# Optimization experiments

Hardware: AMD Instinct MI355X
Metric: run time of the kernel (lower is better)

Reference implementation:

```python
import jax, jax.numpy as jnp
import numpy as np

D_REDUCE = 32
# combination indices (i<j), lexicographic, matching torch.combinations
_IDX_I, _IDX_J = np.triu_indices(D_REDUCE, k=1)


def setup_inputs() -> dict:
    key = jax.random.key(0)
    ks = jax.random.split(key, 5)
    B, L, d_model, d_red = 8, 4096, 1024, D_REDUCE
    plucker_dim = d_red * (d_red - 1) // 2  # 496
    return {
        "h": jax.random.normal(ks[0], (B, L, d_model), dtype=jnp.float32),
        "window_offset": 1,
        "W_red_w": jax.random.normal(ks[1], (d_model, d_red), dtype=jnp.float32) * (1.0 / np.sqrt(d_model)),
        "W_red_b": jax.random.normal(ks[2], (d_red,), dtype=jnp.float32) * 0.01,
        "W_plu_w": jax.random.normal(ks[3], (plucker_dim, d_model), dtype=jnp.float32) * (1.0 / np.sqrt(plucker_dim)),
        "W_plu_b": jax.random.normal(ks[4], (d_model,), dtype=jnp.float32) * 0.01,
    }


def reference(h, window_offset, W_red_w, W_red_b, W_plu_w, W_plu_b):
    B, L, d_model = h.shape
    delta = int(window_offset)
    if delta >= L:
        return jnp.zeros_like(h)
    idx_i = jnp.asarray(_IDX_I)
    idx_j = jnp.asarray(_IDX_J)
    # reduce: (B, L, d_red)
    z = jnp.einsum("bld,dr->blr", h, W_red_w) + W_red_b
    z_t = z[:, delta:, :]        # (B, L-delta, d_red)
    z_td = z[:, : L - delta, :]  # (B, L-delta, d_red)
    # Plucker coordinates: p_ij = z_t[i]*z_td[j] - z_t[j]*z_td[i]  -> (B, L-delta, 496)
    p = z_t[..., idx_i] * z_td[..., idx_j] - z_t[..., idx_j] * z_td[..., idx_i]
    norm = jnp.sqrt(jnp.sum(p * p, axis=-1, keepdims=True))
    p_hat = p / jnp.maximum(norm, 1e-8)
    g_valid = jnp.einsum("blp,pd->bld", p_hat, W_plu_w) + W_plu_b
    g = jnp.zeros((B, L, d_model), dtype=h.dtype)
    g = g.at[:, delta:, :].set(g_valid)
    return g
```

## Files before the change

kernel.cpp:

```cpp
#include <hip/hip_runtime.h>
#include <hip/hip_bf16.h>

#define L_SEQ  4096
#define NBATCH 8
#define DMODEL 1024
#define DRED   32
#define NPAIR  496
#define PK     512
#define MROWS  (NBATCH * L_SEQ)

typedef __bf16 bf16x8 __attribute__((ext_vector_type(8)));
typedef float  f32x4  __attribute__((ext_vector_type(4)));
typedef unsigned short u16x8 __attribute__((ext_vector_type(8)));

typedef const __attribute__((address_space(1))) void g_void;
typedef __attribute__((address_space(3))) void lds_void;

struct PairTab { unsigned short v[512]; };
static constexpr PairTab make_tab() {
  PairTab t{};
  int p = 0;
  for (int i = 0; i < DRED; ++i)
    for (int j = i + 1; j < DRED; ++j) { t.v[p] = (unsigned short)(i | (j << 8)); ++p; }
  for (; p < 512; ++p) t.v[p] = 0;
  return t;
}
__constant__ PairTab PTAB = make_tab();

__global__ __launch_bounds__(256) void ktransW(const float* __restrict__ Wplu,
                                               __bf16* __restrict__ Wt) {
  __shared__ float tile[64][65];
  const int k0 = (blockIdx.x & 7) << 6;
  const int n0 = (blockIdx.x >> 3) << 6;
  const int tid = threadIdx.x;
#pragma unroll
  for (int it = 0; it < 16; ++it) {
    int e = it * 256 + tid;
    int i = e >> 6, j = e & 63;
    float v = 0.f;
    if (k0 + i < NPAIR) v = Wplu[(size_t)(k0 + i) * DMODEL + n0 + j];
    tile[i][j] = v;
  }
  __syncthreads();
#pragma unroll
  for (int it = 0; it < 16; ++it) {
    int e = it * 256 + tid;
    int rn = e >> 6, ck = e & 63;
    Wt[(size_t)(n0 + rn) * PK + k0 + ck] = (__bf16)tile[ck][rn];
  }
}

__global__ __launch_bounds__(256) void kprepWz(const float* __restrict__ Wred,
                                               __bf16* __restrict__ Bh,
                                               __bf16* __restrict__ Bl) {
  int idx = blockIdx.x * 256 + threadIdx.x;
  int n = idx >> 10, k = idx & 1023;
  float v = Wred[k * DRED + n];
  __bf16 hh = (__bf16)v;
  Bh[idx] = hh;
  Bl[idx] = (__bf16)(v - (float)hh);
}

__global__ __launch_bounds__(256) void kz(const float* __restrict__ h,
                                          const __bf16* __restrict__ Bh,
                                          const __bf16* __restrict__ Bl,
                                          const float* __restrict__ Wrb,
                                          float* __restrict__ z) {
  const int w = threadIdx.x >> 6;
  const int lane = threadIdx.x & 63;
  const int l15 = lane & 15, hi = lane >> 4;
  const int m0 = blockIdx.x * 64 + w * 16;
  f32x4 acc[2] = {};
  const float* hp = h + (size_t)(m0 + l15) * DMODEL + hi * 8;
  const __bf16* bh0 = Bh + (size_t)l15 * DMODEL + hi * 8;
  const __bf16* bh1 = bh0 + 16 * DMODEL;
  const __bf16* bl0 = Bl + (size_t)l15 * DMODEL + hi * 8;
  const __bf16* bl1 = bl0 + 16 * DMODEL;
#pragma unroll 8
  for (int kt = 0; kt < 32; ++kt) {
    const int ko = kt * 32;
    f32x4 v0 = *(const f32x4*)(hp + ko);
    f32x4 v1 = *(const f32x4*)(hp + ko + 4);
    bf16x8 ah, al;
#pragma unroll
    for (int q = 0; q < 4; ++q) {
      float f0 = v0[q], f1 = v1[q];
      __bf16 h0 = (__bf16)f0, h1 = (__bf16)f1;
      ah[q] = h0;     ah[q + 4] = h1;
      al[q] = (__bf16)(f0 - (float)h0);
      al[q + 4] = (__bf16)(f1 - (float)h1);
    }
    bf16x8 b0h = *(const bf16x8*)(bh0 + ko);
    bf16x8 b1h = *(const bf16x8*)(bh1 + ko);
    bf16x8 b0l = *(const bf16x8*)(bl0 + ko);
    bf16x8 b1l = *(const bf16x8*)(bl1 + ko);
    acc[0] = __builtin_amdgcn_mfma_f32_16x16x32_bf16(ah, b0h, acc[0], 0, 0, 0);
    acc[1] = __builtin_amdgcn_mfma_f32_16x16x32_bf16(ah, b1h, acc[1], 0, 0, 0);
    acc[0] = __builtin_amdgcn_mfma_f32_16x16x32_bf16(al, b0h, acc[0], 0, 0, 0);
    acc[1] = __builtin_amdgcn_mfma_f32_16x16x32_bf16(al, b1h, acc[1], 0, 0, 0);
    acc[0] = __builtin_amdgcn_mfma_f32_16x16x32_bf16(ah, b0l, acc[0], 0, 0, 0);
    acc[1] = __builtin_amdgcn_mfma_f32_16x16x32_bf16(ah, b1l, acc[1], 0, 0, 0);
  }
#pragma unroll
  for (int nt = 0; nt < 2; ++nt) {
    const float bias = Wrb[nt * 16 + l15];
#pragma unroll
    for (int q = 0; q < 4; ++q) {
      z[(size_t)(m0 + hi * 4 + q) * DRED + nt * 16 + l15] = acc[nt][q] + bias;
    }
  }
}

__global__ __launch_bounds__(256) void kpairs(const float* __restrict__ z,
                                              const int* __restrict__ dOff,
                                              __bf16* __restrict__ A) {
  const int delta = *dOff;
  const int lane = threadIdx.x & 63;
  const int m = blockIdx.x * 4 + (threadIdx.x >> 6);
  const int t = m & (L_SEQ - 1);
  __bf16* arow = A + (size_t)m * PK;
  if (t < delta) {
    u16x8 zz = {0, 0, 0, 0, 0, 0, 0, 0};
    *(u16x8*)(arow + lane * 8) = zz;
    return;
  }
  const float zt  = z[(size_t)m * DRED + (lane & 31)];
  const float ztd = z[(size_t)(m - delta) * DRED + (lane & 31)];
  const u16x8 tab = *(const u16x8*)(PTAB.v + lane * 8);
  float p[8];
  float s = 0.f;
#pragma unroll
  for (int q = 0; q < 8; ++q) {
    const int i = tab[q] & 255;
    const int j = tab[q] >> 8;
    float zti  = __shfl(zt,  i, 64);
    float ztdj = __shfl(ztd, j, 64);
    float ztj  = __shfl(zt,  j, 64);
    float ztdi = __shfl(ztd, i, 64);
    p[q] = fmaf(zti, ztdj, -(ztj * ztdi));
    s = fmaf(p[q], p[q], s);
  }
#pragma unroll
  for (int off = 1; off < 64; off <<= 1) s += __shfl_xor(s, off, 64);
  const float rcp = 1.f / fmaxf(sqrtf(s), 1e-8f);
  bf16x8 o;
#pragma unroll
  for (int q = 0; q < 8; ++q) o[q] = (__bf16)(p[q] * rcp);
  *(bf16x8*)(arow + lane * 8) = o;
}

__global__ __launch_bounds__(256) void kgemm(const __bf16* __restrict__ A,
                                             const __bf16* __restrict__ Bt,
                                             const float* __restrict__ bias,
                                             const int* __restrict__ dOff,
                                             float* __restrict__ out) {
  __shared__ __bf16 Asm[128 * 64];
  __shared__ __bf16 Bsm[128 * 64];
  const int delta = *dOff;
  const int d = blockIdx.x;
  const int lb = ((d & 7) << 8) + (d >> 3);
  const int bm = lb >> 3, bn = lb & 7;
  const int m0 = bm << 7, n0 = bn << 7;
  const int t = threadIdx.x;
  const int wv = t >> 6, lane = t & 63;
  const int l15 = lane & 15, hi = lane >> 4;
  const int wm = (wv >> 1) << 6, wn = (wv & 1) << 6;

  f32x4 acc[4][4] = {};

  for (int kt = 0; kt < 8; ++kt) {
    if (kt) __syncthreads();
    const int kbase = kt * 64;
#pragma unroll
    for (int it = 0; it < 4; ++it) {
      const int c = it * 256 + t;
      const int row = c >> 3, j = c & 7;
      const int jg = j ^ (row & 7);
      const __bf16* ga = A  + (size_t)(m0 + row) * PK + kbase + jg * 8;
      const __bf16* gb = Bt + (size_t)(n0 + row) * PK + kbase + jg * 8;
      char* la = (char*)Asm + (it * 256 + (wv << 6)) * 16;
      char* lbp = (char*)Bsm + (it * 256 + (wv << 6)) * 16;
      __builtin_amdgcn_global_load_lds((g_void*)ga, (lds_void*)la, 16, 0, 0);
      __builtin_amdgcn_global_load_lds((g_void*)gb, (lds_void*)lbp, 16, 0, 0);
    }
    __syncthreads();
#pragma unroll
    for (int kh = 0; kh < 2; ++kh) {
      bf16x8 afr[4], bfr[4];
#pragma unroll
      for (int mi = 0; mi < 4; ++mi) {
        const int row = wm + mi * 16 + l15;
        const int jj = (kh * 4 + hi) ^ (row & 7);
        afr[mi] = *(const bf16x8*)((const char*)Asm + row * 128 + jj * 16);
      }
#pragma unroll
      for (int ni = 0; ni < 4; ++ni) {
        const int row = wn + ni * 16 + l15;
        const int jj = (kh * 4 + hi) ^ (row & 7);
        bfr[ni] = *(const bf16x8*)((const char*)Bsm + row * 128 + jj * 16);
      }
#pragma unroll
      for (int mi = 0; mi < 4; ++mi)
#pragma unroll
        for (int ni = 0; ni < 4; ++ni)
          acc[mi][ni] = __builtin_amdgcn_mfma_f32_16x16x32_bf16(afr[mi], bfr[ni],
                                                                acc[mi][ni], 0, 0, 0);
    }
  }

  float bv[4];
#pragma unroll
  for (int ni = 0; ni < 4; ++ni) bv[ni] = bias[n0 + wn + ni * 16 + l15];
#pragma unroll
  for (int mi = 0; mi < 4; ++mi)
#pragma unroll
    for (int ni = 0; ni < 4; ++ni)
#pragma unroll
      for (int q = 0; q < 4; ++q) {
        const int row = m0 + wm + mi * 16 + hi * 4 + q;
        const int col = n0 + wn + ni * 16 + l15;
        float v = acc[mi][ni][q] + bv[ni];
        if ((row & (L_SEQ - 1)) < delta) v = 0.f;
        out[(size_t)row * DMODEL + col] = v;
      }
}

extern "C" void kernel_launch(void* const* d_in, const int* in_sizes, int n_in,
                              void* d_out, int out_size, void* d_ws, size_t ws_size,
                              hipStream_t stream) {
  const float* h    = (const float*)d_in[0];
  const int*   woff = (const int*)d_in[1];
  const float* Wred = (const float*)d_in[2];
  const float* Wrb  = (const float*)d_in[3];
  const float* Wplu = (const float*)d_in[4];
  const float* Wpb  = (const float*)d_in[5];
  float* out = (float*)d_out;

  char* ws = (char*)d_ws;
  float*  z   = (float*)ws;
  __bf16* Aph = (__bf16*)(ws + (4u << 20));
  __bf16* Wt  = (__bf16*)(ws + (36u << 20));
  __bf16* Bh  = (__bf16*)(ws + (37u << 20));
  __bf16* Bl  = (__bf16*)(ws + (37u << 20) + (64u << 10));

  hipLaunchKernelGGL(ktransW,  dim3(128),        dim3(256), 0, stream, Wplu, Wt);
  hipLaunchKernelGGL(kprepWz,  dim3(128),        dim3(256), 0, stream, Wred, Bh, Bl);
  hipLaunchKernelGGL(kz,       dim3(MROWS / 64), dim3(256), 0, stream, h, Bh, Bl, Wrb, z);
  hipLaunchKernelGGL(kpairs,   dim3(MROWS / 4),  dim3(256), 0, stream, z, woff, Aph);
  hipLaunchKernelGGL(kgemm,    dim3(2048),       dim3(256), 0, stream, Aph, Wt, Wpb, woff, out);
}
```

Measured before the change: 129.4 us.

## Double-buffer GEMM K-tiles in LDS to overlap global loads with MFMA

Splits the K loop of the Plucker GEMM into 32-wide tiles held in two LDS buffers. The next tile is prefetched with global_load_lds while MFMAs run on the current one, and the XOR swizzle is adjusted to the narrower row. This targets load latency that previously stalled each K step, at the cost of twice as many iterations and barriers. A risk is that __syncthreads may not wait on the async LDS loads.

```diff
diff --git a/kernel.cpp b/kernel.cpp
--- a/kernel.cpp
+++ b/kernel.cpp
@@ -154,8 +154,8 @@
                                              const float* __restrict__ bias,
                                              const int* __restrict__ dOff,
                                              float* __restrict__ out) {
-  __shared__ __bf16 Asm[128 * 64];
-  __shared__ __bf16 Bsm[128 * 64];
+  __shared__ __bf16 Asm[2][128 * 32];
+  __shared__ __bf16 Bsm[2][128 * 32];
   const int delta = *dOff;
   const int d = blockIdx.x;
   const int lb = ((d & 7) << 8) + (d >> 3);
@@ -168,45 +168,55 @@
 
   f32x4 acc[4][4] = {};
 
-  for (int kt = 0; kt < 8; ++kt) {
-    if (kt) __syncthreads();
-    const int kbase = kt * 64;
-#pragma unroll
-    for (int it = 0; it < 4; ++it) {
-      const int c = it * 256 + t;
-      const int row = c >> 3, j = c & 7;
-      const int jg = j ^ (row & 7);
-      const __bf16* ga = A  + (size_t)(m0 + row) * PK + kbase + jg * 8;
-      const __bf16* gb = Bt + (size_t)(n0 + row) * PK + kbase + jg * 8;
-      char* la = (char*)Asm + (it * 256 + (wv << 6)) * 16;
-      char* lbp = (char*)Bsm + (it * 256 + (wv << 6)) * 16;
-      __builtin_amdgcn_global_load_lds((g_void*)ga, (lds_void*)la, 16, 0, 0);
-      __builtin_amdgcn_global_load_lds((g_void*)gb, (lds_void*)lbp, 16, 0, 0);
-    }
+  const int r0 = t >> 2,         jsw0 = (t & 3) ^ (r0 & 3);
+  const int r1 = (t + 256) >> 2, jsw1 = (t & 3) ^ (r1 & 3);
+  const __bf16* gA0 = A  + (size_t)(m0 + r0) * PK + jsw0 * 8;
+  const __bf16* gA1 = A  + (size_t)(m0 + r1) * PK + jsw1 * 8;
+  const __bf16* gB0 = Bt + (size_t)(n0 + r0) * PK + jsw0 * 8;
+  const __bf16* gB1 = Bt + (size_t)(n0 + r1) * PK + jsw1 * 8;
+  const int cb0 = (wv << 6) * 16;
+  const int cb1 = (256 + (wv << 6)) * 16;
+
+#define STAGE(buf, kt) do {                                                          \
+    const int _ko = (kt) * 32;                                                       \
+    __builtin_amdgcn_global_load_lds((g_void*)(gA0 + _ko),                           \
+        (lds_void*)((char*)Asm[buf] + cb0), 16, 0, 0);                               \
+    __builtin_amdgcn_global_load_lds((g_void*)(gA1 + _ko),                           \
+        (lds_void*)((char*)Asm[buf] + cb1), 16, 0, 0);                               \
+    __builtin_amdgcn_global_load_lds((g_void*)(gB0 + _ko),                           \
+        (lds_void*)((char*)Bsm[buf] + cb0), 16, 0, 0);                               \
+    __builtin_amdgcn_global_load_lds((g_void*)(gB1 + _ko),                           \
+        (lds_void*)((char*)Bsm[buf] + cb1), 16, 0, 0);                               \
+  } while (0)
+
+  STAGE(0, 0);
+  __syncthreads();
+  int buf = 0;
+  for (int kt = 0; kt < 16; ++kt) {
+    if (kt < 15) STAGE(buf ^ 1, kt + 1);
+    bf16x8 afr[4], bfr[4];
+#pragma unroll
+    for (int mi = 0; mi < 4; ++mi) {
+      const int row = wm + mi * 16 + l15;
+      const int jj = hi ^ (row & 3);
+      afr[mi] = *(const bf16x8*)((const char*)Asm[buf] + row * 64 + jj * 16);
+    }
+#pragma unroll
+    for (int ni = 0; ni < 4; ++ni) {
+      const int row = wn + ni * 16 + l15;
+      const int jj = hi ^ (row & 3);
+      bfr[ni] = *(const bf16x8*)((const char*)Bsm[buf] + row * 64 + jj * 16);
+    }
+#pragma unroll
+    for (int mi = 0; mi < 4; ++mi)
+#pragma unroll
+      for (int ni = 0; ni < 4; ++ni)
+        acc[mi][ni] = __builtin_amdgcn_mfma_f32_16x16x32_bf16(afr[mi], bfr[ni],
+                                                              acc[mi][ni], 0, 0, 0);
     __syncthreads();
-#pragma unroll
-    for (int kh = 0; kh < 2; ++kh) {
-      bf16x8 afr[4], bfr[4];
-#pragma unroll
-      for (int mi = 0; mi < 4; ++mi) {
-        const int row = wm + mi * 16 + l15;
-        const int jj = (kh * 4 + hi) ^ (row & 7);
-        afr[mi] = *(const bf16x8*)((const char*)Asm + row * 128 + jj * 16);
-      }
-#pragma unroll
-      for (int ni = 0; ni < 4; ++ni) {
-        const int row = wn + ni * 16 + l15;
-        const int jj = (kh * 4 + hi) ^ (row & 7);
-        bfr[ni] = *(const bf16x8*)((const char*)Bsm + row * 128 + jj * 16);
-      }
-#pragma unroll
-      for (int mi = 0; mi < 4; ++mi)
-#pragma unroll
-        for (int ni = 0; ni < 4; ++ni)
-          acc[mi][ni] = __builtin_amdgcn_mfma_f32_16x16x32_bf16(afr[mi], bfr[ni],
-                                                                acc[mi][ni], 0, 0, 0);
-    }
-  }
+    buf ^= 1;
+  }
+#undef STAGE
 
   float bv[4];
 #pragma unroll
```

Result: slower. 132.9 us (+2.7%).

## Double-buffer LDS tiles in GEMM to overlap global loads with MFMA

Applied to the files above, without the earlier changes.

Splits the A/B shared-memory tiles into two buffers and prefetches the next K-tile with global_load_lds while MFMAs run on the current one. Uses explicit vmcnt waits and s_barrier in place of __syncthreads around each stage, and precomputes global pointers and LDS offsets outside the loop. This is meant to hide global-memory latency in the K loop, at the cost of doubling LDS use (64KB per block), which may reduce occupancy.

```diff
diff --git a/kernel.cpp b/kernel.cpp
--- a/kernel.cpp
+++ b/kernel.cpp
@@ -154,8 +154,8 @@
                                              const float* __restrict__ bias,
                                              const int* __restrict__ dOff,
                                              float* __restrict__ out) {
-  __shared__ __bf16 Asm[128 * 64];
-  __shared__ __bf16 Bsm[128 * 64];
+  __shared__ __bf16 Asm[2][128 * 64];
+  __shared__ __bf16 Bsm[2][128 * 64];
   const int delta = *dOff;
   const int d = blockIdx.x;
   const int lb = ((d & 7) << 8) + (d >> 3);
@@ -168,22 +168,39 @@
 
   f32x4 acc[4][4] = {};
 
+  const __bf16* gA[4];
+  const __bf16* gB[4];
+  int cb[4];
+#pragma unroll
+  for (int it = 0; it < 4; ++it) {
+    const int c = it * 256 + t;
+    const int row = c >> 3, j = t & 7;
+    const int jg = j ^ (row & 7);
+    gA[it] = A  + (size_t)(m0 + row) * PK + jg * 8;
+    gB[it] = Bt + (size_t)(n0 + row) * PK + jg * 8;
+    cb[it] = (it * 256 + (wv << 6)) * 16;
+  }
+
+#define STAGE(buf, kt) do {                                                      \
+    const int _ko = (kt) * 64;                                                   \
+    _Pragma("unroll")                                                            \
+    for (int _it = 0; _it < 4; ++_it) {                                          \
+      __builtin_amdgcn_global_load_lds((g_void*)(gA[_it] + _ko),                 \
+          (lds_void*)((char*)Asm[buf] + cb[_it]), 16, 0, 0);                     \
+      __builtin_amdgcn_global_load_lds((g_void*)(gB[_it] + _ko),                 \
+          (lds_void*)((char*)Bsm[buf] + cb[_it]), 16, 0, 0);                     \
+    }                                                                            \
+  } while (0)
+
+  STAGE(0, 0);
+#pragma unroll
   for (int kt = 0; kt < 8; ++kt) {
-    if (kt) __syncthreads();
-    const int kbase = kt * 64;
-#pragma unroll
-    for (int it = 0; it < 4; ++it) {
-      const int c = it * 256 + t;
-      const int row = c >> 3, j = c & 7;
-      const int jg = j ^ (row & 7);
-      const __bf16* ga = A  + (size_t)(m0 + row) * PK + kbase + jg * 8;
-      const __bf16* gb = Bt + (size_t)(n0 + row) * PK + kbase + jg * 8;
-      char* la = (char*)Asm + (it * 256 + (wv << 6)) * 16;
-      char* lbp = (char*)Bsm + (it * 256 + (wv << 6)) * 16;
-      __builtin_amdgcn_global_load_lds((g_void*)ga, (lds_void*)la, 16, 0, 0);
-      __builtin_amdgcn_global_load_lds((g_void*)gb, (lds_void*)lbp, 16, 0, 0);
-    }
-    __syncthreads();
+    const int buf = kt & 1;
+    if (kt < 7) STAGE(buf ^ 1, kt + 1);
+    if (kt < 7) asm volatile("s_waitcnt vmcnt(8)" ::: "memory");
+    else        asm volatile("s_waitcnt vmcnt(0)" ::: "memory");
+    __builtin_amdgcn_s_barrier();
+    __builtin_amdgcn_sched_barrier(0);
 #pragma unroll
     for (int kh = 0; kh < 2; ++kh) {
       bf16x8 afr[4], bfr[4];
@@ -191,13 +208,13 @@
       for (int mi = 0; mi < 4; ++mi) {
         const int row = wm + mi * 16 + l15;
         const int jj = (kh * 4 + hi) ^ (row & 7);
-        afr[mi] = *(const bf16x8*)((const char*)Asm + row * 128 + jj * 16);
+        afr[mi] = *(const bf16x8*)((const char*)Asm[buf] + row * 128 + jj * 16);
       }
 #pragma unroll
       for (int ni = 0; ni < 4; ++ni) {
         const int row = wn + ni * 16 + l15;
         const int jj = (kh * 4 + hi) ^ (row & 7);
-        bfr[ni] = *(const bf16x8*)((const char*)Bsm + row * 128 + jj * 16);
+        bfr[ni] = *(const bf16x8*)((const char*)Bsm[buf] + row * 128 + jj * 16);
       }
 #pragma unroll
       for (int mi = 0; mi < 4; ++mi)
@@ -206,7 +223,12 @@
           acc[mi][ni] = __builtin_amdgcn_mfma_f32_16x16x32_bf16(afr[mi], bfr[ni],
                                                                 acc[mi][ni], 0, 0, 0);
     }
-  }
+    if (kt < 7) {
+      asm volatile("" ::: "memory");
+      __builtin_amdgcn_s_barrier();
+    }
+  }
+#undef STAGE
 
   float bv[4];
 #pragma unroll
```

Result: faster. 126.1 us (-2.5%).
